# Optimization experiments

Hardware: AMD Instinct MI355X
Metric: run time of the kernel (lower is better)

## Reference

```python
import jax, jax.numpy as jnp
import numpy as np

B, C_IN, C_OUT, K, H, W_DIM, F_IN = 16, 64, 64, 3, 128, 128, 16
NKW = C_OUT * C_IN * K * K  # 36864 kernel weights per sample


def setup_inputs() -> dict:
    key = jax.random.key(0)
    ks = jax.random.split(key, 8)
    s = 0.05
    return {
        "x": jax.random.normal(ks[0], (B, C_IN, H, W_DIM), dtype=jnp.float32),
        "z": jax.random.normal(ks[1], (B, F_IN), dtype=jnp.float32),
        "W0": jax.random.normal(ks[2], (20, F_IN), dtype=jnp.float32) * s,
        "b0": jax.random.normal(ks[3], (20,), dtype=jnp.float32) * s,
        "W1": jax.random.normal(ks[4], (30, 20), dtype=jnp.float32) * s,
        "b1": jax.random.normal(ks[5], (30,), dtype=jnp.float32) * s,
        "W2": jax.random.normal(ks[6], (NKW + C_OUT, 30), dtype=jnp.float32) * s,
        "b2": jax.random.normal(ks[7], (NKW + C_OUT,), dtype=jnp.float32) * s,
    }


def reference(x, z, W0, b0, W1, b1, W2, b2):
    # Manifold MLP: ReLU after EVERY layer, including the final one (as in original code).
    h = jax.nn.relu(z @ W0.T + b0)
    h = jax.nn.relu(h @ W1.T + b1)
    aw = jax.nn.relu(h @ W2.T + b2)  # [B, NKW + C_OUT]

    kernels = aw[:, :NKW].reshape(B, C_OUT, C_IN, K, K)  # per-sample OIHW kernels
    biases = aw[:, NKW:]  # [B, C_OUT]

    def conv_one(xi, wi, bi):
        # xi: [C_IN, H, W], wi: [C_OUT, C_IN, K, K], bi: [C_OUT]
        y = jax.lax.conv_general_dilated(
            xi[None], wi, window_strides=(1, 1), padding="SAME",
            dimension_numbers=("NCHW", "OIHW", "NCHW"))[0]
        return y + bi[:, None, None]

    out = jax.vmap(conv_one)(x, kernels, biases)  # [B, C_OUT, H, W]
    return jax.nn.relu(out)
```

## Files before the change

kernel.cpp:

```cpp
#include <hip/hip_runtime.h>


typedef __bf16 bf16;
typedef __bf16 bf16x8 __attribute__((ext_vector_type(8)));
typedef float f32x4 __attribute__((ext_vector_type(4)));

#define NB 16
#define CI 64
#define CO 64
#define HH 128
#define WW 128
#define TS 16
#define HALO 18
#define NPL (HALO * HALO)
#define NKW 36864
#define NROWS 36928
#define XHW 130
#define WT2_BYTES ((size_t)NB * 9 * 4096 * 2)
#define BIAS_BYTES 4096
#define XH_BYTES ((size_t)NB * XHW * XHW * CI * 2)
#define WS_NEED (WT2_BYTES + BIAS_BYTES + XH_BYTES)

typedef const __attribute__((address_space(1))) void* gas_ptr;
typedef __attribute__((address_space(3))) void* las_ptr;

__global__ __launch_bounds__(256)
void prep_kernel(const float* __restrict__ x, const float* __restrict__ z,
                 const float* __restrict__ W0, const float* __restrict__ b0,
                 const float* __restrict__ W1, const float* __restrict__ b1,
                 const float* __restrict__ W2, const float* __restrict__ b2,
                 bf16* __restrict__ wt2, float* __restrict__ biases,
                 bf16* __restrict__ xh) {
  const int tid = threadIdx.x;
  if (blockIdx.x < 145) {
    __shared__ float h1s[NB][30];
    if (tid < NB) {
      float h0[20];
      #pragma unroll
      for (int i = 0; i < 20; ++i) {
        float s = b0[i];
        #pragma unroll
        for (int j = 0; j < 16; ++j) s += W0[i * 16 + j] * z[tid * 16 + j];
        h0[i] = fmaxf(s, 0.f);
      }
      #pragma unroll
      for (int i = 0; i < 30; ++i) {
        float s = b1[i];
        #pragma unroll
        for (int j = 0; j < 20; ++j) s += W1[i * 20 + j] * h0[j];
        h1s[tid][i] = fmaxf(s, 0.f);
      }
    }
    __syncthreads();
    const int r = blockIdx.x * 256 + tid;
    if (r >= NROWS) return;
    float w2r[30];
    #pragma unroll
    for (int j = 0; j < 30; ++j) w2r[j] = W2[r * 30 + j];
    const float bb = b2[r];
    const bool isk = r < NKW;
    size_t base = 0;
    if (isk) {
      const int co = r / 576;
      const int rem = r - co * 576;
      const int ci = rem / 9;
      const int tap = rem - ci * 9;
      const int g = co >> 4, mm = co & 15;
      const int kh = ci >> 5, qq = (ci >> 3) & 3, jj = ci & 7;
      base = (size_t)(tap * 8 + g * 2 + kh) * 512 + (size_t)(qq * 16 + mm) * 8 + jj;
    }
    for (int b = 0; b < NB; ++b) {
      float s = bb;
      #pragma unroll
      for (int j = 0; j < 30; ++j) s += w2r[j] * h1s[b][j];
      s = fmaxf(s, 0.f);
      if (isk)
        wt2[(size_t)b * (9 * 4096) + base] = (bf16)s;
      else
        biases[b * CO + (r - NKW)] = s;
    }
    return;
  }

  const int bi = blockIdx.x - 145;
  const int b = bi / XHW;
  const int yp = bi - b * XHW;
  bf16* row = xh + ((size_t)(b * XHW + yp)) * XHW * CI;
  const bf16x8 zero8 = {};
  if (yp == 0 || yp == XHW - 1) {
    for (int g = tid; g < XHW * 8; g += 256)
      *reinterpret_cast<bf16x8*>(row + g * 8) = zero8;
    return;
  }
  if (tid < 8)
    *reinterpret_cast<bf16x8*>(row + tid * 8) = zero8;
  else if (tid >= 248)
    *reinterpret_cast<bf16x8*>(row + (XHW - 1) * CI + (tid - 248) * 8) = zero8;

  const int px = tid & 127;
  const int c0 = (tid >> 7) * 32;
  const float* src =
      x + (((size_t)b * CI + c0) << 14) + ((size_t)(yp - 1) << 7) + px;
  bf16x8 v[4];
  #pragma unroll
  for (int g = 0; g < 4; ++g)
    #pragma unroll
    for (int j = 0; j < 8; ++j)
      v[g][j] = (bf16)src[((size_t)(g * 8 + j)) << 14];
  bf16* dst = row + (px + 1) * CI + c0;
  #pragma unroll
  for (int g = 0; g < 4; ++g)
    *reinterpret_cast<bf16x8*>(dst + g * 8) = v[g];
}

__global__ __launch_bounds__(512, 4)
void conv_kernel(const bf16* __restrict__ xh, const bf16* __restrict__ wt2,
                 const float* __restrict__ bias, float* __restrict__ out) {
  __shared__ __align__(16) bf16 wts[9 * 4096];

  const int id = (blockIdx.x & 7) * 128 + (blockIdx.x >> 3);
  const int b = id >> 6;
  const int x0 = (id & 7) * TS;
  const int y0 = ((id >> 3) & 7) * TS;

  const int tid = threadIdx.x;
  const int lane = tid & 63;
  const int wv = tid >> 6;
  const int m = lane & 15;
  const int q = lane >> 4;

  {
    const bf16* g = wt2 + (size_t)b * (9 * 4096);
    #pragma unroll
    for (int k = 0; k < 9; ++k) {
      const int off = (k * 512 + wv * 64) * 8;
      __builtin_amdgcn_global_load_lds((gas_ptr)(g + off + lane * 8),
                                       (las_ptr)(wts + off), 16, 0, 0);
    }
  }

  const int ty0 = wv * 2;
  const bf16* xb = xh + (((size_t)b * XHW + (y0 + ty0)) * XHW + (x0 + m)) * CI +
                   q * 8;
  const bf16* rp[4];
  #pragma unroll
  for (int r = 0; r < 4; ++r) rp[r] = xb + (size_t)r * XHW * CI;

  f32x4 acc[4][2];
  #pragma unroll
  for (int i = 0; i < 4; ++i) {
    acc[i][0] = (f32x4){0.f, 0.f, 0.f, 0.f};
    acc[i][1] = (f32x4){0.f, 0.f, 0.f, 0.f};
  }

  bf16x8 bb[2][2][2];
  #pragma unroll
  for (int kh = 0; kh < 2; ++kh)
    #pragma unroll
    for (int j = 0; j < 2; ++j)
      bb[0][kh][j] = *reinterpret_cast<const bf16x8*>(rp[j] + kh * 32);

  __syncthreads();

  #pragma unroll
  for (int tap = 0; tap < 9; ++tap) {
    const int cur = tap & 1, nxt = cur ^ 1;
    if (tap < 8) {
      const int dyn = (tap + 1) / 3, dxn = (tap + 1) - dyn * 3;
      #pragma unroll
      for (int kh = 0; kh < 2; ++kh)
        #pragma unroll
        for (int j = 0; j < 2; ++j)
          bb[nxt][kh][j] = *reinterpret_cast<const bf16x8*>(
              rp[j + dyn] + dxn * 64 + kh * 32);
    }
    bf16x8 a[4][2];
    #pragma unroll
    for (int i = 0; i < 4; ++i)
      #pragma unroll
      for (int kh = 0; kh < 2; ++kh)
        a[i][kh] = *reinterpret_cast<const bf16x8*>(
            wts + tap * 4096 + (i * 2 + kh) * 512 + lane * 8);
    __builtin_amdgcn_s_setprio(1);
    #pragma unroll
    for (int kh = 0; kh < 2; ++kh)
      #pragma unroll
      for (int j = 0; j < 2; ++j)
        #pragma unroll
        for (int i = 0; i < 4; ++i)
          acc[i][j] = __builtin_amdgcn_mfma_f32_16x16x32_bf16(
              a[i][kh], bb[cur][kh][j], acc[i][j], 0, 0, 0);
    __builtin_amdgcn_s_setprio(0);
  }

  const float* bp = bias + b * CO;
  float* ob = out + ((size_t)(b * CO) << 14) + (size_t)((y0 + ty0) * WW + x0 + m);
  #pragma unroll
  for (int i = 0; i < 4; ++i)
    #pragma unroll
    for (int j = 0; j < 2; ++j)
      #pragma unroll
      for (int r = 0; r < 4; ++r) {
        const int co = i * 16 + q * 4 + r;
        float v = acc[i][j][r] + bp[co];
        ob[((size_t)co << 14) + j * WW] = fmaxf(v, 0.f);
      }
}

__global__ __launch_bounds__(512, 4)
void conv_fb(const float* __restrict__ x, const bf16* __restrict__ wt2,
             const float* __restrict__ bias, float* __restrict__ out) {
  __shared__ __align__(16) bf16 xt[NPL * 64];

  const int id = (blockIdx.x & 7) * 128 + (blockIdx.x >> 3);
  const int b = id >> 6;
  const int x0 = (id & 7) * TS;
  const int y0 = ((id >> 3) & 7) * TS;

  const int tid = threadIdx.x;
  const int lane = tid & 63;
  const int wv = tid >> 6;
  const int m = lane & 15;
  const int q = lane >> 4;

  const char* wbase = (const char*)wt2 + (size_t)b * (9 * 8192) + lane * 16;

  bf16x8 abuf[2][4][2];
  #pragma unroll
  for (int i = 0; i < 4; ++i)
    #pragma unroll
    for (int kh = 0; kh < 2; ++kh)
      abuf[0][i][kh] =
          *reinterpret_cast<const bf16x8*>(wbase + (i * 2 + kh) * 1024);

  const float* xb = x + ((size_t)b << 20);
  for (int t = 0; t < 6; ++t) {
    const int it = min(tid + t * 512, NPL * 8 - 1);
    const int cig = ((it >> 2) * 810) >> 16;
    const int pl = it - cig * 324;
    const int py = (pl * 57) >> 10;
    const int px = pl - py * 18;
    int gy = y0 + py - 1, gx = x0 + px - 1;
    const bool inb = ((unsigned)gy < (unsigned)HH) & ((unsigned)gx < (unsigned)WW);
    gy = min(max(gy, 0), HH - 1);
    gx = min(max(gx, 0), WW - 1);
    const float* src = xb + ((size_t)cig << 17) + (gy << 7) + gx;
    bf16x8 v8;
    #pragma unroll
    for (int j = 0; j < 8; ++j)
      v8[j] = inb ? (bf16)src[(size_t)j << 14] : (bf16)0.f;
    if (!(t == 5 && tid >= NPL * 8 - 5 * 512))
      *reinterpret_cast<bf16x8*>(reinterpret_cast<char*>(xt) + (pl << 7) +
                                 ((cig ^ (pl & 7)) << 4)) = v8;
  }

  f32x4 acc[4][2];
  #pragma unroll
  for (int i = 0; i < 4; ++i) {
    acc[i][0] = (f32x4){0.f, 0.f, 0.f, 0.f};
    acc[i][1] = (f32x4){0.f, 0.f, 0.f, 0.f};
  }
  const int ty0 = wv * 2;
  __syncthreads();

  #pragma unroll
  for (int tap = 0; tap < 9; ++tap) {
    const int cur = tap & 1, nxt = cur ^ 1;
    if (tap < 8) {
      const char* wt_n = wbase + (tap + 1) * 8192;
      #pragma unroll
      for (int i = 0; i < 4; ++i)
        #pragma unroll
        for (int kh = 0; kh < 2; ++kh)
          abuf[nxt][i][kh] =
              *reinterpret_cast<const bf16x8*>(wt_n + (i * 2 + kh) * 1024);
    }
    const int dy = (tap * 11) >> 5;
    const int dx = tap - dy * 3;
    const int plb = (ty0 + dy) * 18 + dx + m;
    __builtin_amdgcn_s_setprio(1);
    #pragma unroll
    for (int kh = 0; kh < 2; ++kh) {
      const int qk = q + kh * 4;
      #pragma unroll
      for (int j = 0; j < 2; ++j) {
        const int pl = plb + j * 18;
        const bf16x8 bv = *reinterpret_cast<const bf16x8*>(
            reinterpret_cast<const char*>(xt) + (pl << 7) +
            ((qk ^ (pl & 7)) << 4));
        #pragma unroll
        for (int i = 0; i < 4; ++i)
          acc[i][j] = __builtin_amdgcn_mfma_f32_16x16x32_bf16(
              abuf[cur][i][kh], bv, acc[i][j], 0, 0, 0);
      }
    }
    __builtin_amdgcn_s_setprio(0);
  }

  const float* bp = bias + b * CO;
  float* ob = out + ((size_t)(b * CO) << 14) + (size_t)((y0 + ty0) * WW + x0 + m);
  #pragma unroll
  for (int i = 0; i < 4; ++i)
    #pragma unroll
    for (int j = 0; j < 2; ++j)
      #pragma unroll
      for (int r = 0; r < 4; ++r) {
        const int co = i * 16 + q * 4 + r;
        float v = acc[i][j][r] + bp[co];
        ob[((size_t)co << 14) + j * WW] = fmaxf(v, 0.f);
      }
}

extern "C" void kernel_launch(void* const* d_in, const int* in_sizes, int n_in,
                              void* d_out, int out_size, void* d_ws,
                              size_t ws_size, hipStream_t stream) {
  const float* x = (const float*)d_in[0];
  const float* z = (const float*)d_in[1];
  const float* W0 = (const float*)d_in[2];
  const float* b0 = (const float*)d_in[3];
  const float* W1 = (const float*)d_in[4];
  const float* b1 = (const float*)d_in[5];
  const float* W2 = (const float*)d_in[6];
  const float* b2 = (const float*)d_in[7];
  float* out = (float*)d_out;

  bf16* wt2 = (bf16*)d_ws;
  float* biases = (float*)((char*)d_ws + WT2_BYTES);
  bf16* xh = (bf16*)((char*)d_ws + WT2_BYTES + BIAS_BYTES);

  if (ws_size >= WS_NEED) {
    hipLaunchKernelGGL(prep_kernel, dim3(145 + NB * XHW), dim3(256), 0, stream,
                       x, z, W0, b0, W1, b1, W2, b2, wt2, biases, xh);
    hipLaunchKernelGGL(conv_kernel, dim3(1024), dim3(512), 0, stream, xh, wt2,
                       biases, out);
  } else {
    hipLaunchKernelGGL(prep_kernel, dim3(145), dim3(256), 0, stream, x, z, W0,
                       b0, W1, b1, W2, b2, wt2, biases, xh);
    hipLaunchKernelGGL(conv_fb, dim3(1024), dim3(512), 0, stream, x, wt2,
                       biases, out);
  }
}
```

Before: 174.6 us.

## Stage input halo tile in LDS and stream weights from global in conv kernel

The conv kernel used to stage the per-sample weights (72 KB) in LDS and read the input patches straight from global memory. It now loads the 18x18x64 bf16 input halo tile into LDS with an XOR swizzle via global_load_lds, and double-buffers the per-tap weight fragments in registers from global. Shrinking LDS from about 72 KB to about 41 KB should allow more resident blocks and lets the nine taps reuse input data from LDS. In exchange, weight fragments are reloaded from global (mostly L2) by every block, and register use goes up.

```diff
diff --git a/kernel.cpp b/kernel.cpp
--- a/kernel.cpp
+++ b/kernel.cpp
@@ -116,7 +116,7 @@
 __global__ __launch_bounds__(512, 4)
 void conv_kernel(const bf16* __restrict__ xh, const bf16* __restrict__ wt2,
                  const float* __restrict__ bias, float* __restrict__ out) {
-  __shared__ __align__(16) bf16 wts[9 * 4096];
+  __shared__ __align__(16) bf16 xt[2624 * 8];
 
   const int id = (blockIdx.x & 7) * 128 + (blockIdx.x >> 3);
   const int b = id >> 6;
@@ -129,22 +129,41 @@
   const int m = lane & 15;
   const int q = lane >> 4;
 
+  const char* wbase = (const char*)wt2 + (size_t)b * 73728 + lane * 16;
+
+  bf16x8 abuf[2][4][2];
+  #pragma unroll
+  for (int i = 0; i < 4; ++i)
+    #pragma unroll
+    for (int kh = 0; kh < 2; ++kh)
+      abuf[0][i][kh] =
+          *reinterpret_cast<const bf16x8*>(wbase + (i * 2 + kh) * 1024);
+
   {
-    const bf16* g = wt2 + (size_t)b * (9 * 4096);
-    #pragma unroll
-    for (int k = 0; k < 9; ++k) {
-      const int off = (k * 512 + wv * 64) * 8;
-      __builtin_amdgcn_global_load_lds((gas_ptr)(g + off + lane * 8),
-                                       (las_ptr)(wts + off), 16, 0, 0);
-    }
-  }
-
-  const int ty0 = wv * 2;
-  const bf16* xb = xh + (((size_t)b * XHW + (y0 + ty0)) * XHW + (x0 + m)) * CI +
-                   q * 8;
-  const bf16* rp[4];
-  #pragma unroll
-  for (int r = 0; r < 4; ++r) rp[r] = xb + (size_t)r * XHW * CI;
+    const char* xb =
+        (const char*)xh + (((size_t)(b * XHW + y0)) * XHW + x0) * 128;
+    #pragma unroll
+    for (int k = 0; k < 5; ++k) {
+      const int e = k * 512 + tid;
+      const int pl = e >> 3;
+      const int gs = (e & 7) ^ (pl & 7);
+      const int py = (pl * 57) >> 10;
+      const int px = pl - py * 18;
+      __builtin_amdgcn_global_load_lds(
+          (gas_ptr)(xb + ((py * XHW + px) << 7) + (gs << 4)),
+          (las_ptr)((char*)xt + ((k * 512 + wv * 64) << 4)), 16, 0, 0);
+    }
+    if (wv == 0) {
+      const int esrc = min(2560 + lane, 2591);
+      const int pl = esrc >> 3;
+      const int gs = (esrc & 7) ^ (pl & 7);
+      const int py = (pl * 57) >> 10;
+      const int px = pl - py * 18;
+      __builtin_amdgcn_global_load_lds(
+          (gas_ptr)(xb + ((py * XHW + px) << 7) + (gs << 4)),
+          (las_ptr)((char*)xt + (2560 << 4)), 16, 0, 0);
+    }
+  }
 
   f32x4 acc[4][2];
   #pragma unroll
@@ -153,12 +172,7 @@
     acc[i][1] = (f32x4){0.f, 0.f, 0.f, 0.f};
   }
 
-  bf16x8 bb[2][2][2];
-  #pragma unroll
-  for (int kh = 0; kh < 2; ++kh)
-    #pragma unroll
-    for (int j = 0; j < 2; ++j)
-      bb[0][kh][j] = *reinterpret_cast<const bf16x8*>(rp[j] + kh * 32);
+  const int ty0 = wv * 2;
 
   __syncthreads();
 
@@ -166,30 +180,33 @@
   for (int tap = 0; tap < 9; ++tap) {
     const int cur = tap & 1, nxt = cur ^ 1;
     if (tap < 8) {
-      const int dyn = (tap + 1) / 3, dxn = (tap + 1) - dyn * 3;
-      #pragma unroll
-      for (int kh = 0; kh < 2; ++kh)
-        #pragma unroll
-        for (int j = 0; j < 2; ++j)
-          bb[nxt][kh][j] = *reinterpret_cast<const bf16x8*>(
-              rp[j + dyn] + dxn * 64 + kh * 32);
-    }
-    bf16x8 a[4][2];
-    #pragma unroll
-    for (int i = 0; i < 4; ++i)
-      #pragma unroll
-      for (int kh = 0; kh < 2; ++kh)
-        a[i][kh] = *reinterpret_cast<const bf16x8*>(
-            wts + tap * 4096 + (i * 2 + kh) * 512 + lane * 8);
+      const char* wt_n = wbase + (tap + 1) * 8192;
+      #pragma unroll
+      for (int i = 0; i < 4; ++i)
+        #pragma unroll
+        for (int kh = 0; kh < 2; ++kh)
+          abuf[nxt][i][kh] =
+              *reinterpret_cast<const bf16x8*>(wt_n + (i * 2 + kh) * 1024);
+    }
+    const int dy = (tap * 11) >> 5;
+    const int dx = tap - dy * 3;
+    const int plb = (ty0 + dy) * 18 + dx + m;
     __builtin_amdgcn_s_setprio(1);
     #pragma unroll
-    for (int kh = 0; kh < 2; ++kh)
-      #pragma unroll
-      for (int j = 0; j < 2; ++j)
+    for (int kh = 0; kh < 2; ++kh) {
+      const int qk = q + kh * 4;
+      #pragma unroll
+      for (int j = 0; j < 2; ++j) {
+        const int pl = plb + j * 18;
+        const bf16x8 bv = *reinterpret_cast<const bf16x8*>(
+            reinterpret_cast<const char*>(xt) + (pl << 7) +
+            ((qk ^ (pl & 7)) << 4));
         #pragma unroll
         for (int i = 0; i < 4; ++i)
           acc[i][j] = __builtin_amdgcn_mfma_f32_16x16x32_bf16(
-              a[i][kh], bb[cur][kh][j], acc[i][j], 0, 0, 0);
+              abuf[cur][i][kh], bv, acc[i][j], 0, 0, 0);
+      }
+    }
     __builtin_amdgcn_s_setprio(0);
   }
 
@@ -223,7 +240,7 @@
   const int m = lane & 15;
   const int q = lane >> 4;
 
-  const char* wbase = (const char*)wt2 + (size_t)b * (9 * 8192) + lane * 16;
+  const char* wbase = (const char*)wt2 + (size_t)b * 73728 + lane * 16;
 
   bf16x8 abuf[2][4][2];
   #pragma unroll
```

Result: faster. 164.6 us (-5.7%).
